# Kernel tuning notes

Measured on AMD Instinct MI355X. Metric: run time of the kernel, lower is better.

## Reference

```python
import jax, jax.numpy as jnp
import numpy as np

DIM = 128
N_CONV = 4
N_GRAPHS = 256
EPS = 1e-5


def _layernorm(h, g, b):
    m = jnp.mean(h, axis=-1, keepdims=True)
    v = jnp.mean((h - m) ** 2, axis=-1, keepdims=True)
    return g * (h - m) / jnp.sqrt(v + 1e-5) + b


def _gated_gcn(x, ei, e, Wsrc, bsrc, Wdst, bdst, We, be, nxg, nxb, neg, neb):
    # x: [N, D] node feats, ei: [2, E], e: [E, D] edge feats
    n = x.shape[0]
    i, j = ei[0], ei[1]
    sig = jax.nn.sigmoid(e)                                   # [E, D]
    e_sum = jax.ops.segment_sum(sig, i, num_segments=n)       # [N, D]
    e_gated = sig / (e_sum[i] + EPS)                          # [E, D]
    msg = e_gated * (x[j] @ Wdst + bdst)                      # [E, D]
    agg = jax.ops.segment_sum(msg, i, num_segments=n)         # [N, D]
    out = x @ Wsrc + bsrc + agg
    out = x + jax.nn.silu(_layernorm(out, nxg, nxb))
    z = jnp.concatenate([x[i], x[j], e], axis=-1)             # [E, 3D]
    e_new = e + jax.nn.silu(_layernorm(z @ We + be, neg, neb))
    return out, e_new


def setup_inputs() -> dict:
    key = jax.random.key(0)
    ks = iter(jax.random.split(key, 64))
    d = DIM

    def rn(shape, s=0.05):
        return (jax.random.normal(next(ks), shape, dtype=jnp.float32) * s)

    inp = {}
    inp["x"] = jax.random.normal(next(ks), (20000, 92), dtype=jnp.float32)
    inp["edge_attr"] = jax.random.normal(next(ks), (320000, 50), dtype=jnp.float32)
    inp["edge_attr_line"] = jax.random.normal(next(ks), (600000, 40), dtype=jnp.float32)
    inp["edge_index"] = jax.random.randint(next(ks), (2, 320000), 0, 20000, dtype=jnp.int64)
    inp["edge_index_line"] = jax.random.randint(next(ks), (2, 600000), 0, 320000, dtype=jnp.int64)
    inp["batch"] = jnp.sort(jax.random.randint(next(ks), (20000,), 0, N_GRAPHS, dtype=jnp.int64))

    inp["pre1_W"] = rn((92, d)); inp["pre1_b"] = jnp.zeros((d,), jnp.float32)
    inp["pre2_W"] = rn((50, d)); inp["pre2_b"] = jnp.zeros((d,), jnp.float32)
    inp["pre3_W"] = rn((40, d)); inp["pre3_b"] = jnp.zeros((d,), jnp.float32)

    for pfx in ("line", "atom"):
        inp[pfx + "_Wsrc"] = rn((N_CONV, d, d)); inp[pfx + "_bsrc"] = jnp.zeros((N_CONV, d), jnp.float32)
        inp[pfx + "_Wdst"] = rn((N_CONV, d, d)); inp[pfx + "_bdst"] = jnp.zeros((N_CONV, d), jnp.float32)
        inp[pfx + "_We"] = rn((N_CONV, 3 * d, d)); inp[pfx + "_be"] = jnp.zeros((N_CONV, d), jnp.float32)
        inp[pfx + "_nxg"] = jnp.ones((N_CONV, d), jnp.float32); inp[pfx + "_nxb"] = jnp.zeros((N_CONV, d), jnp.float32)
        inp[pfx + "_neg"] = jnp.ones((N_CONV, d), jnp.float32); inp[pfx + "_neb"] = jnp.zeros((N_CONV, d), jnp.float32)

    inp["bn_g"] = jnp.ones((d,), jnp.float32); inp["bn_b"] = jnp.zeros((d,), jnp.float32)
    inp["post_W"] = rn((d, d)); inp["post_b"] = jnp.zeros((d,), jnp.float32)
    inp["out_W"] = rn((d, 1)); inp["out_b"] = jnp.zeros((1,), jnp.float32)
    return inp


def reference(x, edge_attr, edge_attr_line,
              pre1_W, pre1_b, pre2_W, pre2_b, pre3_W, pre3_b,
              line_Wsrc, line_bsrc, line_Wdst, line_bdst, line_We, line_be,
              line_nxg, line_nxb, line_neg, line_neb,
              atom_Wsrc, atom_bsrc, atom_Wdst, atom_bdst, atom_We, atom_be,
              atom_nxg, atom_nxb, atom_neg, atom_neb,
              bn_g, bn_b, post_W, post_b, out_W, out_b,
              edge_index, edge_index_line, batch):
    act = jax.nn.silu
    # pre-FC (single layer each)
    h_node = act(x @ pre1_W + pre1_b)              # [N, D]
    h_edge = act(edge_attr @ pre2_W + pre2_b)      # [E, D]
    h_line = act(edge_attr_line @ pre3_W + pre3_b) # [E_line, D]

    for l in range(N_CONV):
        # line graph conv: nodes = atom edges, edges = line-graph edges
        h_edge, h_line = _gated_gcn(h_edge, edge_index_line, h_line,
                                    line_Wsrc[l], line_bsrc[l], line_Wdst[l], line_bdst[l],
                                    line_We[l], line_be[l],
                                    line_nxg[l], line_nxb[l], line_neg[l], line_neb[l])
        # atom graph conv
        h_node, h_edge = _gated_gcn(h_node, edge_index, h_edge,
                                    atom_Wsrc[l], atom_bsrc[l], atom_Wdst[l], atom_bdst[l],
                                    atom_We[l], atom_be[l],
                                    atom_nxg[l], atom_nxb[l], atom_neg[l], atom_neb[l])
        # dropout_rate = 0 -> identity

    # BatchNorm1d (batch statistics over nodes)
    m = jnp.mean(h_node, axis=0)
    v = jnp.mean((h_node - m) ** 2, axis=0)
    out = bn_g * (h_node - m) / jnp.sqrt(v + 1e-5) + bn_b
    out = act(out)
    out = act(out @ post_W + post_b)

    # global mean pool over crystals
    sums = jax.ops.segment_sum(out, batch, num_segments=N_GRAPHS)
    cnts = jax.ops.segment_sum(jnp.ones((out.shape[0],), out.dtype), batch, num_segments=N_GRAPHS)
    pooled = sums / jnp.maximum(cnts, 1.0)[:, None]
    return (pooled @ out_W + out_b).reshape(-1)    # [N_GRAPHS]
```

## Files before the change

kernel.cpp:

```cpp
#include <hip/hip_runtime.h>

#define NCONV_DEF 4
#define SCH 1024

typedef unsigned short u16;
typedef __attribute__((ext_vector_type(8))) short s8v;
typedef __attribute__((ext_vector_type(4))) float f4v;
typedef __attribute__((ext_vector_type(8))) unsigned short u16x8;

__device__ __forceinline__ float sigm_f(float x){ return 1.f/(1.f+__expf(-x)); }
__device__ __forceinline__ float silu_f(float x){ return x/(1.f+__expf(-x)); }
__device__ __forceinline__ float b2f(u16 h){ union{unsigned u; float f;} v; v.u=(unsigned)h<<16; return v.f; }
__device__ __forceinline__ u16 f2b(float f){ union{float f; unsigned u;} v; v.f=f; unsigned r=v.u+0x7fffu+((v.u>>16)&1u); return (u16)(r>>16); }
__device__ __forceinline__ float ldAv(const float* p, size_t i){ return p[i]; }
__device__ __forceinline__ float ldAv(const u16* p, size_t i){ return b2f(p[i]); }

#define EPS_ 136

__global__ __launch_bounds__(256) void zero_f_k(float* p, long n){
    long i=(long)blockIdx.x*256+threadIdx.x, st=(long)gridDim.x*256;
    for(;i<n;i+=st) p[i]=0.f;
}
__global__ __launch_bounds__(256) void zero_i_k(int* p, long n){
    long i=(long)blockIdx.x*256+threadIdx.x, st=(long)gridDim.x*256;
    for(;i<n;i+=st) p[i]=0;
}
__global__ void diag_k(float* out, int n, float v){
    int i=blockIdx.x*256+threadIdx.x; if(i<n) out[i]=v;
}
__global__ void probe_k(const int* ei, const int* eil, const int* batch, int nb, int* flag){
    if(threadIdx.x||blockIdx.x) return;
    int a=2,b=2,c=2;
    for(int k=0;k<64;k++){ if(ei[2*k+1]!=0) a=1; if(eil[2*k+1]!=0) b=1; }
    int base=nb-128;
    for(int k=0;k<64;k++){ if(batch[base+2*k+1]!=0) c=1; }
    flag[0]=a; flag[1]=b; flag[2]=c;
}

__global__ __launch_bounds__(256)
void hist_k(const int* __restrict__ idx, const int* __restrict__ iflag, int fi,
            int* __restrict__ cnt, int Ne, int Nn){
    int e=blockIdx.x*256+threadIdx.x; if(e>=Ne) return;
    int st=iflag[fi];
    int i=idx[(size_t)e*st]; i=i<0?0:(i>=Nn?Nn-1:i);
    atomicAdd(&cnt[i],1);
}
__global__ __launch_bounds__(256)
void scan1_k(const int* cnt, int* tot, int n){
    __shared__ int sh[256];
    int base=blockIdx.x*SCH, s=0;
    for(int t=threadIdx.x;t<SCH;t+=256){ int i=base+t; s+=(i<n)?cnt[i]:0; }
    sh[threadIdx.x]=s; __syncthreads();
    for(int o=128;o;o>>=1){ if(threadIdx.x<o) sh[threadIdx.x]+=sh[threadIdx.x+o]; __syncthreads(); }
    if(threadIdx.x==0) tot[blockIdx.x]=sh[0];
}
__global__ void scan2_k(int* tot, int nb){
    if(threadIdx.x==0&&blockIdx.x==0){ int acc=0; for(int i=0;i<nb;i++){int v=tot[i]; tot[i]=acc; acc+=v;} }
}
__global__ __launch_bounds__(256)
void scan3_k(const int* cnt, const int* tot, int* off, int n, int total){
    __shared__ int sh[256];
    int b=blockIdx.x, t4=b*SCH+threadIdx.x*4;
    int v0=(t4+0<n)?cnt[t4+0]:0, v1=(t4+1<n)?cnt[t4+1]:0;
    int v2=(t4+2<n)?cnt[t4+2]:0, v3=(t4+3<n)?cnt[t4+3]:0;
    int ls=v0+v1+v2+v3;
    sh[threadIdx.x]=ls; __syncthreads();
    for(int o=1;o<256;o<<=1){
        int val=(threadIdx.x>=o)?sh[threadIdx.x-o]:0; __syncthreads();
        sh[threadIdx.x]+=val; __syncthreads();
    }
    int excl=sh[threadIdx.x]-ls+tot[b];
    if(t4+0<n) off[t4+0]=excl;
    if(t4+1<n) off[t4+1]=excl+v0;
    if(t4+2<n) off[t4+2]=excl+v0+v1;
    if(t4+3<n) off[t4+3]=excl+v0+v1+v2;
    if(b==(int)gridDim.x-1&&threadIdx.x==255) off[n]=total;
}
__global__ __launch_bounds__(256)
void fill_k(const int* __restrict__ idx, const int* __restrict__ iflag, int fi, long joff,
            const int* __restrict__ off, int* __restrict__ cur,
            int* __restrict__ list, int* __restrict__ jlist, int Ne, int Nn){
    int e=blockIdx.x*256+threadIdx.x; if(e>=Ne) return;
    int st=iflag[fi];
    int i=idx[(size_t)e*st]; i=i<0?0:(i>=Nn?Nn-1:i);
    int j=idx[((size_t)joff+e)*st]; j=j<0?0:(j>=Nn?Nn-1:j);
    int pos=off[i]+atomicAdd(&cur[i],1);
    list[pos]=e; jlist[pos]=j;
}

__global__ __launch_bounds__(256)
void pack_w_k(const float* __restrict__ W, u16* __restrict__ Wp, int K, int Kp){
    int i=blockIdx.x*256+threadIdx.x;
    if(i>=128*Kp) return;
    int n=i/Kp, k=i-n*Kp;
    Wp[i] = (k<K) ? f2b(W[(size_t)k*128+n]) : (u16)0;
}

template<typename TA, int ACT>
__global__ __launch_bounds__(256)
void gemm_k(const TA* __restrict__ A, int lda, int M, int K, int Kp,
            const u16* __restrict__ Wp, const float* __restrict__ bias,
            u16* __restrict__ C)
{
    __shared__ __align__(16) u16 As[64*72];
    __shared__ __align__(16) u16 Bs[128*72];
    const int tid=threadIdx.x, row0=blockIdx.x*64;
    const int w=tid>>6, l=tid&63, lr=l&15, kg=l>>4;
    f4v zz={0.f,0.f,0.f,0.f};
    f4v acc[8];
#pragma unroll
    for(int i=0;i<8;++i) acc[i]=zz;

    for(int kt=0;kt<Kp;kt+=64){
        {
            int r=tid>>2, c0=(tid&3)*16;
            int gr=row0+r;
            bool vec=false;
            if constexpr (sizeof(TA)==2) vec=((K&63)==0);
            if(vec){
                const u16* src=(const u16*)(const void*)A+(size_t)gr*lda+kt+c0;
                u16x8 v0={0,0,0,0,0,0,0,0}, v1={0,0,0,0,0,0,0,0};
                if(gr<M){ v0=*(const u16x8*)src; v1=*(const u16x8*)(src+8); }
                *(u16x8*)&As[r*72+c0]=v0;
                *(u16x8*)&As[r*72+c0+8]=v1;
            } else {
                for(int c=c0;c<c0+16;++c){
                    int k=kt+c;
                    float v=(gr<M&&k<K)?ldAv(A,(size_t)gr*lda+k):0.f;
                    As[r*72+c]=f2b(v);
                }
            }
        }
        {
            int n=tid>>1, k0=(tid&1)*32;
            const u16* src=Wp+(size_t)n*Kp+kt+k0;
            *(u16x8*)&Bs[n*72+k0]   =*(const u16x8*)(src);
            *(u16x8*)&Bs[n*72+k0+8] =*(const u16x8*)(src+8);
            *(u16x8*)&Bs[n*72+k0+16]=*(const u16x8*)(src+16);
            *(u16x8*)&Bs[n*72+k0+24]=*(const u16x8*)(src+24);
        }
        __syncthreads();
        const int arow=w*16+lr;
#pragma unroll
        for(int kk=0;kk<64;kk+=32){
            s8v a=*(const s8v*)&As[arow*72+kk+kg*8];
#pragma unroll
            for(int ct=0;ct<8;++ct){
                s8v bfr=*(const s8v*)&Bs[(ct*16+lr)*72+kk+kg*8];
                acc[ct]=__builtin_amdgcn_mfma_f32_16x16x32_bf16(a,bfr,acc[ct],0,0,0);
            }
        }
        __syncthreads();
    }
    u16* ep=Bs;
#pragma unroll
    for(int ct=0;ct<8;++ct){
        int col=ct*16+lr;
        float bv=bias?bias[col]:0.f;
#pragma unroll
        for(int reg=0;reg<4;++reg){
            float v=acc[ct][reg]+bv;
            if(ACT) v=silu_f(v);
            ep[(w*16+kg*4+reg)*EPS_+col]=f2b(v);
        }
    }
    __syncthreads();
    {
        int ar=tid>>2, gr=row0+ar;
        if(gr<M){
            u16* crow=C+(size_t)gr*128+(tid&3)*32;
            const u16* hrow=&ep[ar*EPS_+(tid&3)*32];
#pragma unroll
            for(int c4=0;c4<4;++c4)
                *(u16x8*)(crow+c4*8)=*(const u16x8*)(hrow+c4*8);
        }
    }
}

__global__ __launch_bounds__(256)
void gemmz_k(u16* __restrict__ X, int M,
             const u16* __restrict__ Wp, const float* __restrict__ bias,
             const u16* __restrict__ U,
             const float* __restrict__ g, const float* __restrict__ b)
{
    __shared__ __align__(16) u16 As[2][64*68];
    __shared__ __align__(16) u16 Bs[128*136];
    const int tid=threadIdx.x, row0=blockIdx.x*64;
    const int w=tid>>6, l=tid&63, lr=l&15, kg=l>>4;
    u16* ep=&As[0][0];
    const int ar=tid>>2, gr=row0+ar;
    {
        u16x8 z8={0,0,0,0,0,0,0,0};
        u16x8 u0=z8,u1=z8,u2=z8,u3=z8;
        if(gr<M){
            const u16* ur=U+(size_t)gr*128+(tid&3)*32;
            u0=*(const u16x8*)(ur); u1=*(const u16x8*)(ur+8);
            u2=*(const u16x8*)(ur+16); u3=*(const u16x8*)(ur+24);
        }
        u16* d=&ep[ar*EPS_+(tid&3)*32];
        *(u16x8*)(d)=u0; *(u16x8*)(d+8)=u1; *(u16x8*)(d+16)=u2; *(u16x8*)(d+24)=u3;
    }
    __syncthreads();
    f4v acc[8];
#pragma unroll
    for(int ct=0;ct<8;++ct){
        int col=ct*16+lr;
        float bv=bias[col];
#pragma unroll
        for(int reg=0;reg<4;++reg)
            acc[ct][reg]=b2f(ep[(w*16+kg*4+reg)*EPS_+col])+bv;
    }
    __syncthreads();

    {
        int c0=(tid&3)*16;
        const u16* src=X+(size_t)gr*128;
        u16x8 z8={0,0,0,0,0,0,0,0};
        u16x8 v0=z8,v1=z8,v2=z8,v3=z8;
        if(gr<M){
            v0=*(const u16x8*)(src+c0);    v1=*(const u16x8*)(src+c0+8);
            v2=*(const u16x8*)(src+64+c0); v3=*(const u16x8*)(src+64+c0+8);
        }
        *(u16x8*)&As[0][ar*68+c0]=v0;  *(u16x8*)&As[0][ar*68+c0+8]=v1;
        *(u16x8*)&As[1][ar*68+c0]=v2;  *(u16x8*)&As[1][ar*68+c0+8]=v3;
        int bn=tid>>1, bk=(tid&1)*64;
        const u16* wsrc=Wp+(size_t)bn*128+bk;
#pragma unroll
        for(int q=0;q<8;++q)
            *(u16x8*)&Bs[bn*136+bk+q*8]=*(const u16x8*)(wsrc+q*8);
    }
    __syncthreads();
    const int arow=w*16+lr;
#pragma unroll
    for(int kt=0;kt<2;++kt){
#pragma unroll
        for(int kk=0;kk<64;kk+=32){
            s8v a=*(const s8v*)&As[kt][arow*68+kk+kg*8];
#pragma unroll
            for(int ct=0;ct<8;++ct){
                s8v bfr=*(const s8v*)&Bs[(ct*16+lr)*136+kt*64+kk+kg*8];
                acc[ct]=__builtin_amdgcn_mfma_f32_16x16x32_bf16(a,bfr,acc[ct],0,0,0);
            }
        }
    }
    float sum[4]={0.f,0.f,0.f,0.f}, sq[4]={0.f,0.f,0.f,0.f};
#pragma unroll
    for(int ct=0;ct<8;++ct)
#pragma unroll
        for(int reg=0;reg<4;++reg){
            float v=acc[ct][reg];
            sum[reg]+=v; sq[reg]+=v*v;
        }
#pragma unroll
    for(int m=1;m<16;m<<=1)
#pragma unroll
        for(int reg=0;reg<4;++reg){
            sum[reg]+=__shfl_xor(sum[reg],m,64);
            sq[reg] +=__shfl_xor(sq[reg], m,64);
        }
    float mean[4], rstd[4];
#pragma unroll
    for(int reg=0;reg<4;++reg){
        mean[reg]=sum[reg]*(1.f/128.f);
        float var=sq[reg]*(1.f/128.f)-mean[reg]*mean[reg];
        rstd[reg]=rsqrtf(var+1e-5f);
    }
    __syncthreads();
#pragma unroll
    for(int ct=0;ct<8;++ct){
        int col=ct*16+lr;
        float gv=g[col], bv=b[col];
#pragma unroll
        for(int reg=0;reg<4;++reg){
            float h=gv*(acc[ct][reg]-mean[reg])*rstd[reg]+bv;
            ep[(w*16+kg*4+reg)*EPS_+col]=f2b(silu_f(h));
        }
    }
    if(gr<M){
        u16* xrow=X+(size_t)gr*128+(tid&3)*32;
        const u16* hrow=&ep[ar*EPS_+(tid&3)*32];
#pragma unroll
        for(int c4=0;c4<4;++c4){
            u16x8 xv=*(const u16x8*)(xrow+c4*8);
            u16x8 hv=*(const u16x8*)(hrow+c4*8);
            u16x8 ov;
#pragma unroll
            for(int j=0;j<8;++j) ov[j]=f2b(b2f(xv[j])+b2f(hv[j]));
            *(u16x8*)(xrow+c4*8)=ov;
        }
    }
}

template<int FIN, int HASPREV>
__global__ __launch_bounds__(256)
void gather_k(const u16* __restrict__ e, const u16* __restrict__ P1,
              u16* __restrict__ U,
              const int* __restrict__ off, const int* __restrict__ list,
              const int* __restrict__ jlist,
              int Nn, int c0, int c1)
{
    int wid=threadIdx.x>>6, lane=threadIdx.x&63;
    int n=blockIdx.x*4+wid; if(n>=Nn) return;
    int beg=off[n], end=off[n+1];
    float es0=0.f,es1=0.f,a0=0.f,a1=0.f;
    for(int k=beg;k<end;++k){
        int eid=list[k], j=jlist[k];
        bool in=(j>=c0)&&(j<c1);
        if(FIN||in){
            unsigned ev=*(const unsigned*)(e+(size_t)eid*128+2*lane);
            float s0=sigm_f(b2f((u16)(ev&0xffff)));
            float s1=sigm_f(b2f((u16)(ev>>16)));
            if(FIN){ es0+=s0; es1+=s1; }
            if(in){
                unsigned pv=*(const unsigned*)(P1+(size_t)(j-c0)*128+2*lane);
                a0+=s0*b2f((u16)(pv&0xffff));
                a1+=s1*b2f((u16)(pv>>16));
            }
        }
    }
    unsigned* up=(unsigned*)(U+(size_t)n*128+2*lane);
    if(!FIN){
        *up=((unsigned)f2b(a0))|((unsigned)f2b(a1)<<16);
    } else {
        if(HASPREV){
            unsigned pv=*up;
            a0+=b2f((u16)(pv&0xffff));
            a1+=b2f((u16)(pv>>16));
        }
        float r0=1.f/(es0+1e-5f), r1=1.f/(es1+1e-5f);
        *up=((unsigned)f2b(a0*r0))|((unsigned)f2b(a1*r1)<<16);
    }
}

__global__ __launch_bounds__(256)
void edgez_k(u16* __restrict__ e, const u16* __restrict__ x,
             const int* __restrict__ idx, long joff,
             const int* __restrict__ iflag, int fi,
             const u16* __restrict__ Wep, const float* __restrict__ be,
             const float* __restrict__ g, const float* __restrict__ b,
             int Ne, int Nn)
{
    __shared__ __align__(16) u16 As[2][64*68];
    __shared__ __align__(16) u16 Bs[2][128*68];
    __shared__ int rid[128];
    const int tid=threadIdx.x, row0=blockIdx.x*64;
    const int w=tid>>6, l=tid&63, lr=l&15, kg=l>>4;
    int st=iflag[fi];
    if(tid<128){
        int r=tid&63, eid=row0+r; if(eid>=Ne) eid=Ne-1;
        long elem=(tid<64)?(long)eid:(joff+eid);
        int v=idx[(size_t)elem*st]; v=v<0?0:(v>=Nn?Nn-1:v);
        rid[tid]=v;
    }
    __syncthreads();
    const int ar=tid>>2, ac=(tid&3)*16;
    const int bn=tid>>1, bk=(tid&1)*32;
    int eidA=row0+ar; if(eidA>=Ne) eidA=Ne-1;
    const u16* aptr0=x+(size_t)rid[ar]*128;
    const u16* aptr1=x+(size_t)rid[64+ar]*128;
    const u16* aptr2=e+(size_t)eidA*128;

    f4v zz={0.f,0.f,0.f,0.f};
    f4v acc[8];
#pragma unroll
    for(int i=0;i<8;++i) acc[i]=zz;

    u16x8 a0,a1,b0,b1,b2,b3;
    u16x8 er0,er1,er2,er3;
    {
        const u16* src=aptr0+ac;
        a0=*(const u16x8*)src; a1=*(const u16x8*)(src+8);
        const u16* wsrc=Wep+(size_t)bn*384+bk;
        b0=*(const u16x8*)wsrc; b1=*(const u16x8*)(wsrc+8);
        b2=*(const u16x8*)(wsrc+16); b3=*(const u16x8*)(wsrc+24);
    }
#pragma unroll
    for(int s=0;s<6;++s){
        const int buf=s&1;
        *(u16x8*)&As[buf][ar*68+ac]  =a0;
        *(u16x8*)&As[buf][ar*68+ac+8]=a1;
        *(u16x8*)&Bs[buf][bn*68+bk]   =b0;
        *(u16x8*)&Bs[buf][bn*68+bk+8] =b1;
        *(u16x8*)&Bs[buf][bn*68+bk+16]=b2;
        *(u16x8*)&Bs[buf][bn*68+bk+24]=b3;
        if(s<5){
            const int sn=s+1, sec=sn>>1, half=sn&1;
            const u16* src=(sec==0?aptr0:(sec==1?aptr1:aptr2))+half*64+ac;
            a0=*(const u16x8*)src; a1=*(const u16x8*)(src+8);
            if(sec==2){ if(half==0){ er0=a0; er1=a1; } else { er2=a0; er3=a1; } }
            const u16* wsrc=Wep+(size_t)bn*384+sn*64+bk;
            b0=*(const u16x8*)wsrc; b1=*(const u16x8*)(wsrc+8);
            b2=*(const u16x8*)(wsrc+16); b3=*(const u16x8*)(wsrc+24);
        }
        __syncthreads();
        __builtin_amdgcn_s_setprio(1);
        const int arow=w*16+lr;
#pragma unroll
        for(int kk=0;kk<64;kk+=32){
            s8v a=*(const s8v*)&As[buf][arow*68+kk+kg*8];
#pragma unroll
            for(int ct=0;ct<8;++ct){
                s8v bfr=*(const s8v*)&Bs[buf][(ct*16+lr)*68+kk+kg*8];
                acc[ct]=__builtin_amdgcn_mfma_f32_16x16x32_bf16(a,bfr,acc[ct],0,0,0);
            }
        }
        __builtin_amdgcn_s_setprio(0);
    }
    float sum[4]={0.f,0.f,0.f,0.f}, sq[4]={0.f,0.f,0.f,0.f};
#pragma unroll
    for(int ct=0;ct<8;++ct){
        float bev=be[ct*16+lr];
#pragma unroll
        for(int reg=0;reg<4;++reg){
            float v=acc[ct][reg]+bev;
            acc[ct][reg]=v;
            sum[reg]+=v; sq[reg]+=v*v;
        }
    }
#pragma unroll
    for(int m=1;m<16;m<<=1){
#pragma unroll
        for(int reg=0;reg<4;++reg){
            sum[reg]+=__shfl_xor(sum[reg],m,64);
            sq[reg] +=__shfl_xor(sq[reg], m,64);
        }
    }
    float mean[4], rstd[4];
#pragma unroll
    for(int reg=0;reg<4;++reg){
        mean[reg]=sum[reg]*(1.f/128.f);
        float var=sq[reg]*(1.f/128.f)-mean[reg]*mean[reg];
        rstd[reg]=rsqrtf(var+1e-5f);
    }
    u16* ep=&Bs[0][0];
#pragma unroll
    for(int ct=0;ct<8;++ct){
        int col=ct*16+lr;
        float gv=g[col], bv=b[col];
#pragma unroll
        for(int reg=0;reg<4;++reg){
            float h=gv*(acc[ct][reg]-mean[reg])*rstd[reg]+bv;
            ep[(w*16+kg*4+reg)*EPS_+col]=f2b(silu_f(h));
        }
    }
    {
        int eid=row0+ar;
        if(eid<Ne){
            u16* erow=e+(size_t)eid*128;
            const u16* hr=&ep[ar*EPS_];
            u16x8 h0=*(const u16x8*)(hr+ac),    h1=*(const u16x8*)(hr+ac+8);
            u16x8 h2=*(const u16x8*)(hr+64+ac), h3=*(const u16x8*)(hr+64+ac+8);
            u16x8 o0,o1,o2,o3;
#pragma unroll
            for(int j=0;j<8;++j){
                o0[j]=f2b(b2f(er0[j])+b2f(h0[j]));
                o1[j]=f2b(b2f(er1[j])+b2f(h1[j]));
                o2[j]=f2b(b2f(er2[j])+b2f(h2[j]));
                o3[j]=f2b(b2f(er3[j])+b2f(h3[j]));
            }
            *(u16x8*)(erow+ac)=o0;    *(u16x8*)(erow+ac+8)=o1;
            *(u16x8*)(erow+64+ac)=o2; *(u16x8*)(erow+64+ac+8)=o3;
        }
    }
}

__global__ __launch_bounds__(256)
void bn_stats_k(const u16* __restrict__ h, float* __restrict__ st, int N){
    int t=blockIdx.x*256+threadIdx.x;
    int d=t&127, r0=t>>7, rstride=(gridDim.x*256)>>7;
    float s=0.f,q=0.f;
    for(int r=r0;r<N;r+=rstride){ float v=b2f(h[(size_t)r*128+d]); s+=v; q+=v*v; }
    atomicAdd(&st[d],s); atomicAdd(&st[128+d],q);
}
__global__ __launch_bounds__(256)
void bn_apply_k(u16* __restrict__ h, const float* __restrict__ st,
                const float* __restrict__ g, const float* __restrict__ b, int N){
    int t=blockIdx.x*256+threadIdx.x;
    if(t>=N*128) return;
    int d=t&127;
    float inv=1.f/(float)N;
    float m=st[d]*inv, var=st[128+d]*inv-m*m;
    float v=g[d]*(b2f(h[t])-m)*rsqrtf(var+1e-5f)+b[d];
    h[t]=f2b(silu_f(v));
}
__global__ __launch_bounds__(256)
void pool_k(const u16* __restrict__ o, const int* __restrict__ batch,
            const int* __restrict__ iflag,
            float* __restrict__ pooled, float* __restrict__ cnt, int N, int NG){
    int st=iflag[2];
    int wid=threadIdx.x>>6, lane=threadIdx.x&63;
    int n=blockIdx.x*4+wid; if(n>=N) return;
    int gi=batch[(size_t)n*st]; gi=gi<0?0:(gi>=NG?NG-1:gi);
    atomicAdd(&pooled[(size_t)gi*128+lane],    b2f(o[(size_t)n*128+lane]));
    atomicAdd(&pooled[(size_t)gi*128+64+lane], b2f(o[(size_t)n*128+64+lane]));
    if(lane==0) atomicAdd(&cnt[gi],1.f);
}
__global__ void final_k(const float* __restrict__ pooled, const float* __restrict__ cnt,
                        const float* __restrict__ oW, const float* __restrict__ ob,
                        float* __restrict__ out){
    int gi=blockIdx.x, lane=threadIdx.x;
    float v=pooled[(size_t)gi*128+lane]*oW[lane]
           +pooled[(size_t)gi*128+64+lane]*oW[64+lane];
    for(int m=32;m;m>>=1) v+=__shfl_xor(v,m,64);
    if(lane==0) out[gi]=v/fmaxf(cnt[gi],1.f)+ob[0];
}

template<typename TA>
static inline void gemm(hipStream_t s, const TA* A, int lda, int M, int K, int Kp,
                        const u16* Wp, const float* bias, u16* C, int act){
    dim3 grid((M+63)/64);
    if(act) gemm_k<TA,1><<<grid,256,0,s>>>(A,lda,M,K,Kp,Wp,bias,C);
    else    gemm_k<TA,0><<<grid,256,0,s>>>(A,lda,M,K,Kp,Wp,bias,C);
}

static inline void build_csr(hipStream_t s, const int* idx, int fi, long joff, const int* iflag,
                             int Ne, int Nn, int* off, int* cur, int* list, int* jlist, int* tot){
    int nb=(Nn+SCH-1)/SCH;
    zero_i_k<<<256,256,0,s>>>(cur,Nn);
    hist_k<<<(Ne+255)/256,256,0,s>>>(idx,iflag,fi,cur,Ne,Nn);
    scan1_k<<<nb,256,0,s>>>(cur,tot,Nn);
    scan2_k<<<1,1,0,s>>>(tot,nb);
    scan3_k<<<nb,256,0,s>>>(cur,tot,off,Nn,Ne);
    zero_i_k<<<256,256,0,s>>>(cur,Nn);
    fill_k<<<(Ne+255)/256,256,0,s>>>(idx,iflag,fi,joff,off,cur,list,jlist,Ne,Nn);
}

static inline void pack_w(hipStream_t s, const float* W, u16* Wp, int K, int Kp){
    pack_w_k<<<(128*Kp+255)/256,256,0,s>>>(W,Wp,K,Kp);
}

extern "C" void kernel_launch(void* const* d_in, const int* in_sizes, int n_in,
                              void* d_out, int out_size, void* d_ws, size_t ws_size,
                              hipStream_t stream)
{
    const float* x_in =(const float*)d_in[0];
    const float* ea   =(const float*)d_in[1];
    const float* eal  =(const float*)d_in[2];
    const int*   ei   =(const int*)d_in[3];
    const int*   eil  =(const int*)d_in[4];
    const int*   batch=(const int*)d_in[5];
    const float* pre1W=(const float*)d_in[6];  const float* pre1b=(const float*)d_in[7];
    const float* pre2W=(const float*)d_in[8];  const float* pre2b=(const float*)d_in[9];
    const float* pre3W=(const float*)d_in[10]; const float* pre3b=(const float*)d_in[11];
    const float* lWsrc=(const float*)d_in[12]; const float* lbsrc=(const float*)d_in[13];
    const float* lWdst=(const float*)d_in[14]; const float* lbdst=(const float*)d_in[15];
    const float* lWe  =(const float*)d_in[16]; const float* lbe  =(const float*)d_in[17];
    const float* lnxg =(const float*)d_in[18]; const float* lnxb =(const float*)d_in[19];
    const float* lneg =(const float*)d_in[20]; const float* lneb =(const float*)d_in[21];
    const float* aWsrc=(const float*)d_in[22]; const float* absrc=(const float*)d_in[23];
    const float* aWdst=(const float*)d_in[24]; const float* abdst=(const float*)d_in[25];
    const float* aWe  =(const float*)d_in[26]; const float* abe  =(const float*)d_in[27];
    const float* anxg =(const float*)d_in[28]; const float* anxb =(const float*)d_in[29];
    const float* aneg =(const float*)d_in[30]; const float* aneb =(const float*)d_in[31];
    const float* bng  =(const float*)d_in[32]; const float* bnb  =(const float*)d_in[33];
    const float* postW=(const float*)d_in[34]; const float* postb=(const float*)d_in[35];
    const float* outW =(const float*)d_in[36]; const float* outb =(const float*)d_in[37];
    (void)n_in;

    const int N =in_sizes[5];
    const int E =in_sizes[3]/2;
    const int EL=in_sizes[4]/2;
    const int NG=out_size;
    const int CH=(E+1)/2;

    char* base=(char*)d_ws;
    size_t off=0;
    auto alloc=[&](size_t bytes)->char*{
        char* p=base+off; off=(off+bytes+255)&~(size_t)255; return p;
    };
    u16* hN   =(u16*)alloc((size_t)N*128*2);
    u16* hE   =(u16*)alloc((size_t)E*128*2);
    u16* hL   =(u16*)alloc((size_t)EL*128*2);
    u16* U    =(u16*)alloc((size_t)E*128*2);
    u16* P1   =(u16*)alloc((size_t)CH*128*2);
    int* off_l=(int*)alloc((size_t)(E+1)*4);
    int* cur_l=(int*)alloc((size_t)E*4);
    int* list_l=(int*)alloc((size_t)EL*4);
    int* jlist_l=(int*)alloc((size_t)EL*4);
    int* off_a=(int*)alloc((size_t)(N+1)*4);
    int* cur_a=(int*)alloc((size_t)N*4);
    int* list_a=(int*)alloc((size_t)E*4);
    int* jlist_a=(int*)alloc((size_t)E*4);
    int* tot  =(int*)alloc(4096);
    int* iflag=(int*)alloc(64);
    float* stats =(float*)alloc(256*4);
    float* pooled=(float*)alloc((size_t)NG*128*4);
    float* cnt   =(float*)alloc((size_t)NG*4);
    u16* pre1p=(u16*)alloc(128*128*2);
    u16* pre2p=(u16*)alloc(128*64*2);
    u16* pre3p=(u16*)alloc(128*64*2);
    u16* postp=(u16*)alloc(128*128*2);
    u16 *lsrcp[4],*ldstp[4],*lWep[4],*asrcp[4],*adstp[4],*aWep[4];
    for(int i=0;i<4;i++){
        lsrcp[i]=(u16*)alloc(128*128*2);
        ldstp[i]=(u16*)alloc(128*128*2);
        lWep[i] =(u16*)alloc(128*384*2);
        asrcp[i]=(u16*)alloc(128*128*2);
        adstp[i]=(u16*)alloc(128*128*2);
        aWep[i] =(u16*)alloc(128*384*2);
    }
    if(off>ws_size){
        diag_k<<<(NG+255)/256,256,0,stream>>>((float*)d_out,NG,(float)(ws_size>>20)+0.25f);
        return;
    }

    probe_k<<<1,64,0,stream>>>(ei,eil,batch,N,iflag);
    build_csr(stream,eil,1,EL,iflag,EL,E,off_l,cur_l,list_l,jlist_l,tot);
    build_csr(stream,ei, 0,E, iflag,E, N,off_a,cur_a,list_a,jlist_a,tot);

    pack_w(stream,pre1W,pre1p,92,128);
    pack_w(stream,pre2W,pre2p,50,64);
    pack_w(stream,pre3W,pre3p,40,64);
    pack_w(stream,postW,postp,128,128);
    for(int i=0;i<4;i++){
        pack_w(stream,lWsrc+(size_t)i*128*128,lsrcp[i],128,128);
        pack_w(stream,lWdst+(size_t)i*128*128,ldstp[i],128,128);
        pack_w(stream,lWe  +(size_t)i*384*128,lWep[i],384,384);
        pack_w(stream,aWsrc+(size_t)i*128*128,asrcp[i],128,128);
        pack_w(stream,aWdst+(size_t)i*128*128,adstp[i],128,128);
        pack_w(stream,aWe  +(size_t)i*384*128,aWep[i],384,384);
    }

    gemm(stream,x_in,92,N, 92,128,pre1p,pre1b,hN,1);
    gemm(stream,ea,  50,E, 50, 64,pre2p,pre2b,hE,1);
    gemm(stream,eal, 40,EL,40, 64,pre3p,pre3b,hL,1);

    for(int l=0;l<NCONV_DEF;++l){
        {
            gemm(stream,hE,128,CH,128,128,ldstp[l],lbdst+l*128,P1,0);
            gather_k<0,0><<<(E+3)/4,256,0,stream>>>(hL,P1,U,off_l,list_l,jlist_l,E,0,CH);
            gemm(stream,hE+(size_t)CH*128,128,E-CH,128,128,ldstp[l],lbdst+l*128,P1,0);
            gather_k<1,1><<<(E+3)/4,256,0,stream>>>(hL,P1,U,off_l,list_l,jlist_l,E,CH,E);
            edgez_k<<<(EL+63)/64,256,0,stream>>>(hL,hE,eil,EL,iflag,1,
                                                 lWep[l],lbe+l*128,lneg+l*128,lneb+l*128,EL,E);
            gemmz_k<<<(E+63)/64,256,0,stream>>>(hE,E,lsrcp[l],lbsrc+l*128,U,
                                                lnxg+l*128,lnxb+l*128);
        }
        {
            gemm(stream,hN,128,N,128,128,adstp[l],abdst+l*128,P1,0);
            gather_k<1,0><<<(N+3)/4,256,0,stream>>>(hE,P1,U,off_a,list_a,jlist_a,N,0,N);
            edgez_k<<<(E+63)/64,256,0,stream>>>(hE,hN,ei,E,iflag,0,
                                                aWep[l],abe+l*128,aneg+l*128,aneb+l*128,E,N);
            gemmz_k<<<(N+63)/64,256,0,stream>>>(hN,N,asrcp[l],absrc+l*128,U,
                                                anxg+l*128,anxb+l*128);
        }
    }

    zero_f_k<<<64,256,0,stream>>>(stats,256);
    zero_f_k<<<64,256,0,stream>>>(pooled,(long)NG*128);
    zero_f_k<<<1,256,0,stream>>>(cnt,NG);
    bn_stats_k<<<256,256,0,stream>>>(hN,stats,N);
    bn_apply_k<<<(N*128+255)/256,256,0,stream>>>(hN,stats,bng,bnb,N);

    gemm(stream,hN,128,N,128,128,postp,postb,P1,1);

    pool_k<<<(N+3)/4,256,0,stream>>>(P1,batch,iflag,pooled,cnt,N,NG);
    final_k<<<NG,64,0,stream>>>(pooled,cnt,outW,outb,(float*)d_out);
}
```

Before: 3.663 ms.

## Pipeline gather loads with half-wave rows and enlarge edgez tile to 128 rows

The gather kernel now assigns each half-wavefront to one row with 8-byte loads, and it prefetches the next neighbour's edge and message vectors while the current one is being accumulated. This is meant to hide the latency of the dependent gather chain. The edge-update GEMM kernel now uses 512-thread blocks covering 128 edge rows, so each weight tile loaded into shared memory is reused across twice as many rows. It also adds a barrier before the shared buffer is reused in the epilogue. In exchange, the larger shared-memory footprint and block size may lower occupancy.

```diff
diff --git a/kernel.cpp b/kernel.cpp
--- a/kernel.cpp
+++ b/kernel.cpp
@@ -300,39 +300,69 @@
               int Nn, int c0, int c1)
 {
     int wid=threadIdx.x>>6, lane=threadIdx.x&63;
-    int n=blockIdx.x*4+wid; if(n>=Nn) return;
-    int beg=off[n], end=off[n+1];
-    float es0=0.f,es1=0.f,a0=0.f,a1=0.f;
-    for(int k=beg;k<end;++k){
+    int h=lane>>5, sl=lane&31;
+    int n=blockIdx.x*8+wid*2+h;
+    int beg=0,end=0;
+    if(n<Nn){ beg=off[n]; end=off[n+1]; }
+    const int d4=sl*4;
+    uint2 uprev; uprev.x=0; uprev.y=0;
+    if(FIN&&HASPREV&&n<Nn) uprev=*(const uint2*)(U+(size_t)n*128+d4);
+
+    float es[4]={0.f,0.f,0.f,0.f}, a[4]={0.f,0.f,0.f,0.f};
+    int k=beg;
+    uint2 ev_n, pv_n; ev_n.x=ev_n.y=0; pv_n.x=pv_n.y=0;
+    bool in_n=false;
+    if(k<end){
         int eid=list[k], j=jlist[k];
-        bool in=(j>=c0)&&(j<c1);
-        if(FIN||in){
-            unsigned ev=*(const unsigned*)(e+(size_t)eid*128+2*lane);
-            float s0=sigm_f(b2f((u16)(ev&0xffff)));
-            float s1=sigm_f(b2f((u16)(ev>>16)));
-            if(FIN){ es0+=s0; es1+=s1; }
-            if(in){
-                unsigned pv=*(const unsigned*)(P1+(size_t)(j-c0)*128+2*lane);
-                a0+=s0*b2f((u16)(pv&0xffff));
-                a1+=s1*b2f((u16)(pv>>16));
-            }
-        }
-    }
-    unsigned* up=(unsigned*)(U+(size_t)n*128+2*lane);
+        in_n=(j>=c0)&&(j<c1);
+        if(FIN||in_n) ev_n=*(const uint2*)(e+(size_t)eid*128+d4);
+        if(in_n)      pv_n=*(const uint2*)(P1+(size_t)(j-c0)*128+d4);
+    }
+    while(k<end){
+        uint2 ev=ev_n, pv=pv_n; bool in=in_n;
+        int kn=k+1;
+        if(kn<end){
+            int eid=list[kn], j=jlist[kn];
+            in_n=(j>=c0)&&(j<c1);
+            ev_n.x=ev_n.y=0; pv_n.x=pv_n.y=0;
+            if(FIN||in_n) ev_n=*(const uint2*)(e+(size_t)eid*128+d4);
+            if(in_n)      pv_n=*(const uint2*)(P1+(size_t)(j-c0)*128+d4);
+        }
+        float s0=sigm_f(b2f((u16)(ev.x&0xffff)));
+        float s1=sigm_f(b2f((u16)(ev.x>>16)));
+        float s2=sigm_f(b2f((u16)(ev.y&0xffff)));
+        float s3=sigm_f(b2f((u16)(ev.y>>16)));
+        if(FIN){ es[0]+=s0; es[1]+=s1; es[2]+=s2; es[3]+=s3; }
+        if(in){
+            a[0]+=s0*b2f((u16)(pv.x&0xffff));
+            a[1]+=s1*b2f((u16)(pv.x>>16));
+            a[2]+=s2*b2f((u16)(pv.y&0xffff));
+            a[3]+=s3*b2f((u16)(pv.y>>16));
+        }
+        k=kn;
+    }
+    if(n>=Nn) return;
+    uint2* up=(uint2*)(U+(size_t)n*128+d4);
+    uint2 o;
     if(!FIN){
-        *up=((unsigned)f2b(a0))|((unsigned)f2b(a1)<<16);
+        o.x=((unsigned)f2b(a[0]))|((unsigned)f2b(a[1])<<16);
+        o.y=((unsigned)f2b(a[2]))|((unsigned)f2b(a[3])<<16);
     } else {
         if(HASPREV){
-            unsigned pv=*up;
-            a0+=b2f((u16)(pv&0xffff));
-            a1+=b2f((u16)(pv>>16));
-        }
-        float r0=1.f/(es0+1e-5f), r1=1.f/(es1+1e-5f);
-        *up=((unsigned)f2b(a0*r0))|((unsigned)f2b(a1*r1)<<16);
-    }
-}
-
-__global__ __launch_bounds__(256)
+            a[0]+=b2f((u16)(uprev.x&0xffff));
+            a[1]+=b2f((u16)(uprev.x>>16));
+            a[2]+=b2f((u16)(uprev.y&0xffff));
+            a[3]+=b2f((u16)(uprev.y>>16));
+        }
+        float r0=1.f/(es[0]+1e-5f), r1=1.f/(es[1]+1e-5f);
+        float r2=1.f/(es[2]+1e-5f), r3=1.f/(es[3]+1e-5f);
+        o.x=((unsigned)f2b(a[0]*r0))|((unsigned)f2b(a[1]*r1)<<16);
+        o.y=((unsigned)f2b(a[2]*r2))|((unsigned)f2b(a[3]*r3)<<16);
+    }
+    *up=o;
+}
+
+__global__ __launch_bounds__(512)
 void edgez_k(u16* __restrict__ e, const u16* __restrict__ x,
              const int* __restrict__ idx, long joff,
              const int* __restrict__ iflag, int fi,
@@ -340,24 +370,24 @@
              const float* __restrict__ g, const float* __restrict__ b,
              int Ne, int Nn)
 {
-    __shared__ __align__(16) u16 As[2][64*68];
+    __shared__ __align__(16) u16 As[2][128*68];
     __shared__ __align__(16) u16 Bs[2][128*68];
-    __shared__ int rid[128];
-    const int tid=threadIdx.x, row0=blockIdx.x*64;
+    __shared__ int rid[256];
+    const int tid=threadIdx.x, row0=blockIdx.x*128;
     const int w=tid>>6, l=tid&63, lr=l&15, kg=l>>4;
     int st=iflag[fi];
-    if(tid<128){
-        int r=tid&63, eid=row0+r; if(eid>=Ne) eid=Ne-1;
-        long elem=(tid<64)?(long)eid:(joff+eid);
+    if(tid<256){
+        int r=tid&127, eid=row0+r; if(eid>=Ne) eid=Ne-1;
+        long elem=(tid<128)?(long)eid:(joff+eid);
         int v=idx[(size_t)elem*st]; v=v<0?0:(v>=Nn?Nn-1:v);
         rid[tid]=v;
     }
     __syncthreads();
     const int ar=tid>>2, ac=(tid&3)*16;
-    const int bn=tid>>1, bk=(tid&1)*32;
+    const int bn=tid>>2, bk=(tid&3)*16;
     int eidA=row0+ar; if(eidA>=Ne) eidA=Ne-1;
     const u16* aptr0=x+(size_t)rid[ar]*128;
-    const u16* aptr1=x+(size_t)rid[64+ar]*128;
+    const u16* aptr1=x+(size_t)rid[128+ar]*128;
     const u16* aptr2=e+(size_t)eidA*128;
 
     f4v zz={0.f,0.f,0.f,0.f};
@@ -365,24 +395,21 @@
 #pragma unroll
     for(int i=0;i<8;++i) acc[i]=zz;
 
-    u16x8 a0,a1,b0,b1,b2,b3;
+    u16x8 a0,a1,b0,b1;
     u16x8 er0,er1,er2,er3;
     {
         const u16* src=aptr0+ac;
         a0=*(const u16x8*)src; a1=*(const u16x8*)(src+8);
         const u16* wsrc=Wep+(size_t)bn*384+bk;
         b0=*(const u16x8*)wsrc; b1=*(const u16x8*)(wsrc+8);
-        b2=*(const u16x8*)(wsrc+16); b3=*(const u16x8*)(wsrc+24);
     }
 #pragma unroll
     for(int s=0;s<6;++s){
         const int buf=s&1;
         *(u16x8*)&As[buf][ar*68+ac]  =a0;
         *(u16x8*)&As[buf][ar*68+ac+8]=a1;
-        *(u16x8*)&Bs[buf][bn*68+bk]   =b0;
-        *(u16x8*)&Bs[buf][bn*68+bk+8] =b1;
-        *(u16x8*)&Bs[buf][bn*68+bk+16]=b2;
-        *(u16x8*)&Bs[buf][bn*68+bk+24]=b3;
+        *(u16x8*)&Bs[buf][bn*68+bk]  =b0;
+        *(u16x8*)&Bs[buf][bn*68+bk+8]=b1;
         if(s<5){
             const int sn=s+1, sec=sn>>1, half=sn&1;
             const u16* src=(sec==0?aptr0:(sec==1?aptr1:aptr2))+half*64+ac;
@@ -390,7 +417,6 @@
             if(sec==2){ if(half==0){ er0=a0; er1=a1; } else { er2=a0; er3=a1; } }
             const u16* wsrc=Wep+(size_t)bn*384+sn*64+bk;
             b0=*(const u16x8*)wsrc; b1=*(const u16x8*)(wsrc+8);
-            b2=*(const u16x8*)(wsrc+16); b3=*(const u16x8*)(wsrc+24);
         }
         __syncthreads();
         __builtin_amdgcn_s_setprio(1);
@@ -432,6 +458,7 @@
         float var=sq[reg]*(1.f/128.f)-mean[reg]*mean[reg];
         rstd[reg]=rsqrtf(var+1e-5f);
     }
+    __syncthreads();
     u16* ep=&Bs[0][0];
 #pragma unroll
     for(int ct=0;ct<8;++ct){
@@ -439,8 +466,8 @@
         float gv=g[col], bv=b[col];
 #pragma unroll
         for(int reg=0;reg<4;++reg){
-            float h=gv*(acc[ct][reg]-mean[reg])*rstd[reg]+bv;
-            ep[(w*16+kg*4+reg)*EPS_+col]=f2b(silu_f(h));
+            float hh=gv*(acc[ct][reg]-mean[reg])*rstd[reg]+bv;
+            ep[(w*16+kg*4+reg)*EPS_+col]=f2b(silu_f(hh));
         }
     }
     {
@@ -628,19 +655,19 @@
     for(int l=0;l<NCONV_DEF;++l){
         {
             gemm(stream,hE,128,CH,128,128,ldstp[l],lbdst+l*128,P1,0);
-            gather_k<0,0><<<(E+3)/4,256,0,stream>>>(hL,P1,U,off_l,list_l,jlist_l,E,0,CH);
+            gather_k<0,0><<<(E+7)/8,256,0,stream>>>(hL,P1,U,off_l,list_l,jlist_l,E,0,CH);
             gemm(stream,hE+(size_t)CH*128,128,E-CH,128,128,ldstp[l],lbdst+l*128,P1,0);
-            gather_k<1,1><<<(E+3)/4,256,0,stream>>>(hL,P1,U,off_l,list_l,jlist_l,E,CH,E);
-            edgez_k<<<(EL+63)/64,256,0,stream>>>(hL,hE,eil,EL,iflag,1,
-                                                 lWep[l],lbe+l*128,lneg+l*128,lneb+l*128,EL,E);
+            gather_k<1,1><<<(E+7)/8,256,0,stream>>>(hL,P1,U,off_l,list_l,jlist_l,E,CH,E);
+            edgez_k<<<(EL+127)/128,512,0,stream>>>(hL,hE,eil,EL,iflag,1,
+                                                   lWep[l],lbe+l*128,lneg+l*128,lneb+l*128,EL,E);
             gemmz_k<<<(E+63)/64,256,0,stream>>>(hE,E,lsrcp[l],lbsrc+l*128,U,
                                                 lnxg+l*128,lnxb+l*128);
         }
         {
             gemm(stream,hN,128,N,128,128,adstp[l],abdst+l*128,P1,0);
-            gather_k<1,0><<<(N+3)/4,256,0,stream>>>(hE,P1,U,off_a,list_a,jlist_a,N,0,N);
-            edgez_k<<<(E+63)/64,256,0,stream>>>(hE,hN,ei,E,iflag,0,
-                                                aWep[l],abe+l*128,aneg+l*128,aneb+l*128,E,N);
+            gather_k<1,0><<<(N+7)/8,256,0,stream>>>(hE,P1,U,off_a,list_a,jlist_a,N,0,N);
+            edgez_k<<<(E+127)/128,512,0,stream>>>(hE,hN,ei,E,iflag,0,
+                                                  aWep[l],abe+l*128,aneg+l*128,aneb+l*128,E,N);
             gemmz_k<<<(N+63)/64,256,0,stream>>>(hN,N,asrcp[l],absrc+l*128,U,
                                                 anxg+l*128,anxb+l*128);
         }
```

After: 3.109 ms (median of 2 runs). 1.18x faster.
